# Kernel optimization log

Hardware: AMD Instinct MI355X
Metric: run time of the kernel (lower is better)

## Reference

```python
import jax, jax.numpy as jnp
import numpy as np

N = 100000
E = 1600000
EMB = 256
D = 128
B = 4096
L = 50
NCLASS = 10


def _spmm(edge_src, edge_dst, edge_w, h):
    # adj @ h with adj given as weighted edge list (dst aggregates from src)
    msg = h[edge_src] * edge_w[:, None]          # [E, D]
    return jax.ops.segment_sum(msg, edge_dst, num_segments=h.shape[0])


def setup_inputs() -> dict:
    key = jax.random.key(0)
    ks = jax.random.split(key, 20)
    inp = {}
    inp["A1_tensor"] = jax.random.normal(ks[0], (N, EMB), dtype=jnp.float32)
    inp["edge_src"] = jax.random.randint(ks[1], (E,), 0, N, dtype=jnp.int32)
    inp["edge_dst"] = jax.random.randint(ks[2], (E,), 0, N, dtype=jnp.int32)
    inp["edge_w"] = jax.random.uniform(ks[3], (E,), dtype=jnp.float32)
    inp["batch_idx"] = jax.random.randint(ks[4], (B, 1, L), 0, N, dtype=jnp.int32)
    s = 0.05  # modest init scale for numerical sanity
    inp["w_gc1"] = jax.random.normal(ks[5], (EMB, D), dtype=jnp.float32) * s
    inp["b_gc1"] = jax.random.normal(ks[6], (D,), dtype=jnp.float32) * s
    inp["w_gc2"] = jax.random.normal(ks[7], (D, D), dtype=jnp.float32) * s
    inp["b_gc2"] = jax.random.normal(ks[8], (D,), dtype=jnp.float32) * s
    inp["n_param"] = jax.random.uniform(ks[9], (N, 1), dtype=jnp.float32)
    inp["Lin1"] = jax.random.normal(ks[10], (EMB, D), dtype=jnp.float32) * s
    inp["Lin1_bias"] = jax.random.normal(ks[11], (D,), dtype=jnp.float32) * s
    inp["weight2"] = jax.random.normal(ks[12], (D, 64), dtype=jnp.float32) * s
    inp["bias2"] = jax.random.normal(ks[13], (64,), dtype=jnp.float32) * s
    inp["lin1_w"] = jax.random.normal(ks[14], ((L + 1) * 64, D), dtype=jnp.float32) * s
    inp["lin1_b"] = jax.random.normal(ks[15], (D,), dtype=jnp.float32) * s
    inp["classifier"] = jax.random.normal(ks[16], (D, NCLASS), dtype=jnp.float32) * s
    inp["classifier_bias"] = jax.random.normal(ks[17], (NCLASS,), dtype=jnp.float32) * s
    return inp


def reference(A1_tensor, edge_src, edge_dst, edge_w, batch_idx,
              w_gc1, b_gc1, w_gc2, b_gc2, n_param, Lin1, Lin1_bias,
              weight2, bias2, lin1_w, lin1_b, classifier, classifier_bias):
    # eval mode: both dropouts are identity
    a0 = A1_tensor @ Lin1 + Lin1_bias              # [N, D]
    a1 = a0 * n_param                              # per-node convex gate
    x1 = _spmm(edge_src, edge_dst, edge_w, A1_tensor @ w_gc1 + b_gc1)  # gc1
    x1 = a1 + x1 * (1.0 - n_param)
    x2 = _spmm(edge_src, edge_dst, edge_w, x1 @ w_gc2 + b_gc2)         # gc2
    bidx = batch_idx[:, 0, :]                      # [B, L]
    sel = x2[bidx]                                 # [B, L, D] irregular gather
    sel = jnp.concatenate([sel, jnp.sum(sel, axis=1, keepdims=True)], axis=1)  # [B, L+1, D]
    sel = jnp.einsum('bld,de->ble', sel, weight2) + bias2                      # [B, L+1, 64]
    sel = sel.reshape(bidx.shape[0], -1)           # [B, (L+1)*64]
    sel = sel @ lin1_w + lin1_b                    # [B, D]
    pre = sel @ classifier + classifier_bias       # [B, nclass]
    return (jnp.argmax(pre, axis=-1), sel)
```

## Files before the change

kernel.cpp:

```cpp
#include <hip/hip_runtime.h>
#include <cstdint>

#define NN   100000
#define EE   1600000
#define EMBD 256
#define DD   128
#define BBB  4096
#define LLL  50
#define NCLS 10

#define NB   196
#define BSH  9
#define EPB  4096

#define FIXS 1048576.0f
#define INVS (1.0f / 1048576.0f)

typedef __attribute__((ext_vector_type(8))) short bf16x8;
typedef __attribute__((ext_vector_type(4))) float f32x4;

__device__ __forceinline__ ushort f2bf(float f) {
  uint32_t u = __float_as_uint(f);
  u += 0x7fffu + ((u >> 16) & 1u);
  return (ushort)(u >> 16);
}
__device__ __forceinline__ float bf2f(ushort h) {
  return __uint_as_float(((uint32_t)h) << 16);
}

template<int BM, int BN, int BK, int TM, int TN>
__global__ __launch_bounds__(256)
void gemm_f32(const float* __restrict__ Av, int lda,
              const float* __restrict__ W, int ldw,
              const float* __restrict__ bias,
              float* __restrict__ Cv, int ldc,
              int M, int ktot, int kper,
              const int* __restrict__ bidxg,
              const float* __restrict__ Sg)
{
  constexpr int TX = BN / TN;
  constexpr int TY = BM / TM;
  static_assert(TX * TY == 256, "thread mapping");
  static_assert(TN % 4 == 0, "epilogue uses 4-wide vectors");
  constexpr int AQ = BK / 4;
  constexpr int ALOADS = (BM * AQ) / 256;
  static_assert((BM * AQ) % 256 == 0, "A-tile load mapping");
  constexpr int WQ4 = BN / 4;
  constexpr int WLOADS = (BK * WQ4) / 256;
  static_assert((BK * WQ4) % 256 == 0, "W-tile load mapping");

  __shared__ float As[BK][BM + 4];
  __shared__ float Ws[BK][BN];

  const int tid = threadIdx.x;
  const int tx = tid % TX, ty = tid / TX;
  const int bm0 = blockIdx.x * BM;
  const int bn0 = blockIdx.y * BN;
  const int z = blockIdx.z;
  const int koff = z * kper;
  int kc = ktot - koff; if (kc > kper) kc = kper;
  W += bn0 + (size_t)koff * ldw;
  Cv += (size_t)z * (size_t)M * ldc;
  const float* biasp = bias ? bias + bn0 : nullptr;

  float acc[TM][TN];
#pragma unroll
  for (int i = 0; i < TM; ++i)
#pragma unroll
    for (int j = 0; j < TN; ++j) acc[i][j] = 0.f;

  for (int kt = 0; kt < kc; kt += BK) {
#pragma unroll
    for (int p = 0; p < ALOADS; ++p) {
      int f = tid + p * 256;
      int row = f / AQ, q = f % AQ;
      int arow = bm0 + row;
      float4 av = make_float4(0.f, 0.f, 0.f, 0.f);
      if (arow < M) {
        if (bidxg) {
          int k = koff + kt + (q << 2);
          int l = k >> 6, jj = k & 63;
          const float* ap = (l < LLL)
              ? (Av + (size_t)bidxg[arow * LLL + l] * 64 + jj)
              : (Sg + (size_t)arow * 64 + jj);
          av = *(const float4*)ap;
        } else {
          av = *(const float4*)(Av + (long long)arow * lda + koff + kt + (q << 2));
        }
      }
      As[(q << 2) + 0][row] = av.x;
      As[(q << 2) + 1][row] = av.y;
      As[(q << 2) + 2][row] = av.z;
      As[(q << 2) + 3][row] = av.w;
    }
#pragma unroll
    for (int p = 0; p < WLOADS; ++p) {
      int f = tid + p * 256;
      int krow = f / WQ4, c4 = f % WQ4;
      *(float4*)&Ws[krow][c4 << 2] =
          *(const float4*)(W + (long long)(kt + krow) * ldw + (c4 << 2));
    }
    __syncthreads();
#pragma unroll
    for (int kk = 0; kk < BK; ++kk) {
      float a[TM], b[TN];
      if constexpr (TM % 4 == 0) {
#pragma unroll
        for (int i = 0; i < TM; i += 4)
          *(float4*)&a[i] = *(const float4*)&As[kk][ty * TM + i];
      } else {
#pragma unroll
        for (int i = 0; i < TM; ++i) a[i] = As[kk][ty * TM + i];
      }
#pragma unroll
      for (int j = 0; j < TN; j += 4)
        *(float4*)&b[j] = *(const float4*)&Ws[kk][tx * TN + j];
#pragma unroll
      for (int i = 0; i < TM; ++i)
#pragma unroll
        for (int j = 0; j < TN; ++j)
          acc[i][j] = fmaf(a[i], b[j], acc[i][j]);
    }
    __syncthreads();
  }

#pragma unroll
  for (int i = 0; i < TM; ++i) {
    int r = bm0 + ty * TM + i;
    if (r >= M) continue;
#pragma unroll
    for (int j4 = 0; j4 < TN; j4 += 4) {
      float4 v = make_float4(acc[i][j4], acc[i][j4 + 1],
                             acc[i][j4 + 2], acc[i][j4 + 3]);
      if (biasp != nullptr) {
        v.x += biasp[tx * TN + j4 + 0]; v.y += biasp[tx * TN + j4 + 1];
        v.z += biasp[tx * TN + j4 + 2]; v.w += biasp[tx * TN + j4 + 3];
      }
      *(float4*)(Cv + (long long)r * ldc + bn0 + tx * TN + j4) = v;
    }
  }
}

__global__ __launch_bounds__(256)
void gemm_qp_mfma(const float* __restrict__ A1,
                  const ushort* __restrict__ Wfh,
                  const ushort* __restrict__ Wfl,
                  const float* __restrict__ bab,
                  float* __restrict__ Qb, float* __restrict__ Pb, int M)
{
  __shared__ ushort LAh[64][32];
  __shared__ ushort LAl[64][32];
  const int tid = threadIdx.x;
  const int w = tid >> 6, l = tid & 63;
  const int bm0 = blockIdx.x * 64;
  const int srow = tid >> 2, skg = tid & 3;
  const int frow = (w << 4) + (l & 15);
  const int fk   = (l >> 4) << 3;

  f32x4 acc[8];
#pragma unroll
  for (int c = 0; c < 8; ++c) acc[c] = (f32x4){0.f, 0.f, 0.f, 0.f};

  for (int kt8 = 0; kt8 < 8; ++kt8) {
    {
      int grow = bm0 + srow;
      float x[8];
      if (grow < M) {
        const float* ap = A1 + (size_t)grow * 256 + (kt8 << 5) + (skg << 3);
        *(float4*)&x[0] = *(const float4*)ap;
        *(float4*)&x[4] = *(const float4*)(ap + 4);
      } else {
#pragma unroll
        for (int j = 0; j < 8; ++j) x[j] = 0.f;
      }
      ushort h[8], lo[8];
#pragma unroll
      for (int j = 0; j < 8; ++j) {
        h[j] = f2bf(x[j]);
        lo[j] = f2bf(x[j] - bf2f(h[j]));
      }
      *(bf16x8*)&LAh[srow][skg << 3] = *(bf16x8*)h;
      *(bf16x8*)&LAl[srow][skg << 3] = *(bf16x8*)lo;
    }
    __syncthreads();

    bf16x8 ah = *(const bf16x8*)&LAh[frow][fk];
    bf16x8 al = *(const bf16x8*)&LAl[frow][fk];
#pragma unroll
    for (int ct = 0; ct < 8; ++ct) {
      size_t off = ((size_t)((kt8 << 3) + ct) * 64 + l) << 3;
      bf16x8 bh = *(const bf16x8*)(Wfh + off);
      bf16x8 bl = *(const bf16x8*)(Wfl + off);
      acc[ct] = __builtin_amdgcn_mfma_f32_16x16x32_bf16(ah, bh, acc[ct], 0, 0, 0);
      acc[ct] = __builtin_amdgcn_mfma_f32_16x16x32_bf16(ah, bl, acc[ct], 0, 0, 0);
      acc[ct] = __builtin_amdgcn_mfma_f32_16x16x32_bf16(al, bh, acc[ct], 0, 0, 0);
    }
    __syncthreads();
  }

  const int r0 = bm0 + (w << 4) + ((l >> 4) << 2);
#pragma unroll
  for (int ct = 0; ct < 8; ++ct) {
    int gcol = (ct << 4) + (l & 15);
    float bia = bab[gcol];
    float* dst = (gcol < 64) ? (Qb + gcol) : (Pb + (gcol - 64));
#pragma unroll
    for (int r = 0; r < 4; ++r) {
      int grow = r0 + r;
      if (grow < M) dst[(size_t)grow * 64] = acc[ct][r] + bia;
    }
  }
}

__global__ __launch_bounds__(256)
void wfrag_k(const float* __restrict__ Wab, ushort* __restrict__ Wfh,
             ushort* __restrict__ Wfl)
{
  int t = blockIdx.x * 256 + threadIdx.x;
  if (t >= 4096) return;
  int f = t >> 6, l = t & 63;
  int kt = f >> 3, ct = f & 7;
  int row0 = (kt << 5) + ((l >> 4) << 3);
  int col = (ct << 4) + (l & 15);
  ushort h[8], lo[8];
#pragma unroll
  for (int j = 0; j < 8; ++j) {
    float x = Wab[(row0 + j) * 128 + col];
    h[j] = f2bf(x);
    lo[j] = f2bf(x - bf2f(h[j]));
  }
  size_t off = ((size_t)t) << 3;
  *(bf16x8*)(Wfh + off) = *(bf16x8*)h;
  *(bf16x8*)(Wfl + off) = *(bf16x8*)lo;
}

__global__ __launch_bounds__(256)
void fuse1_k(const float* __restrict__ wgc1, const float* __restrict__ lin1,
             const float* __restrict__ bgc1, const float* __restrict__ lin1b,
             const float* __restrict__ wgc2,
             float* __restrict__ T1, float* __restrict__ T2,
             float* __restrict__ ta, float* __restrict__ tb)
{
  int t = blockIdx.x * 256 + threadIdx.x;
  const float* Arow; float* outp; int n;
  if (t < 32768)      { n = t & 127; Arow = wgc1 + (t >> 7) * 128; outp = T1 + t; }
  else if (t < 65536) { int u = t - 32768; n = u & 127; Arow = lin1 + (u >> 7) * 128; outp = T2 + u; }
  else if (t < 65664) { n = t - 65536; Arow = bgc1;  outp = ta + n; }
  else if (t < 65792) { n = t - 65664; Arow = lin1b; outp = tb + n; }
  else return;
  float s = 0.f;
  for (int k = 0; k < 128; ++k) s = fmaf(Arow[k], wgc2[k * 128 + n], s);
  *outp = s;
}

__global__ __launch_bounds__(256)
void fuse2_k(const float* __restrict__ T1, const float* __restrict__ T2,
             const float* __restrict__ ta, const float* __restrict__ tb,
             const float* __restrict__ bgc2, const float* __restrict__ w2,
             float* __restrict__ Wab, float* __restrict__ bab,
             float* __restrict__ bcv)
{
  int t = blockIdx.x * 256 + threadIdx.x;
  const float* Arow; float* outp; int j;
  if (t < 32768) {
    int c = t & 127; j = c & 63;
    Arow = (c < 64 ? T1 : T2) + (t >> 7) * 128;
    outp = Wab + t;
  } else if (t < 32896) {
    int c = t - 32768; j = c & 63; Arow = (c < 64) ? ta : tb; outp = bab + c;
  } else if (t < 32960) {
    j = t - 32896; Arow = bgc2; outp = bcv + j;
  } else return;
  float s = 0.f;
  for (int k = 0; k < 128; ++k) s = fmaf(Arow[k], w2[k * 64 + j], s);
  *outp = s;
}

__global__ __launch_bounds__(256)
void cnt_k(const int* __restrict__ edst, int* __restrict__ gbkt)
{
  __shared__ int l[NB];
  const int tid = threadIdx.x;
  for (int i = tid; i < NB; i += 256) l[i] = 0;
  __syncthreads();
  const int e0 = blockIdx.x * EPB;
  const int e1 = min(EE, e0 + EPB);
#pragma unroll
  for (int u = 0; u < 16; ++u) {
    int e = e0 + u * 256 + tid;
    if (e < e1) atomicAdd(&l[edst[e] >> BSH], 1);
  }
  __syncthreads();
  for (int i = tid; i < NB; i += 256)
    if (l[i]) atomicAdd(&gbkt[i], l[i]);
}

__global__ __launch_bounds__(256)
void scanB_k(const int* __restrict__ gbkt, int* __restrict__ bbase,
             int* __restrict__ gcur, int* __restrict__ rp)
{
  __shared__ int s[256];
  int t = threadIdx.x;
  int v = (t < NB) ? gbkt[t] : 0;
  s[t] = v;
  __syncthreads();
  for (int off = 1; off < 256; off <<= 1) {
    int u = (t >= off) ? s[t - off] : 0;
    __syncthreads();
    s[t] += u;
    __syncthreads();
  }
  if (t < NB) {
    int ex = s[t] - v;
    bbase[t] = ex;
    gcur[t] = ex;
  }
  if (t == 0) { bbase[NB] = EE; rp[NN] = EE; }
}

__global__ __launch_bounds__(256)
void bin_k(const int* __restrict__ edst, const int* __restrict__ esrc,
           const float* __restrict__ ew, int* __restrict__ gcur,
           int4* __restrict__ ebd)
{
  __shared__ int lcnt[NB];
  __shared__ int lbase[NB];
  const int tid = threadIdx.x;
  const int e0 = blockIdx.x * EPB;
  const int e1 = min(EE, e0 + EPB);
  for (int i = tid; i < NB; i += 256) lcnt[i] = 0;
  __syncthreads();
  int dv[16], sv[16], wv[16];
#pragma unroll
  for (int u = 0; u < 16; ++u) {
    int e = e0 + u * 256 + tid;
    if (e < e1) {
      dv[u] = edst[e];
      sv[u] = esrc[e];
      wv[u] = __float_as_int(ew[e]);
      atomicAdd(&lcnt[dv[u] >> BSH], 1);
    } else dv[u] = -1;
  }
  __syncthreads();
  for (int i = tid; i < NB; i += 256) {
    lbase[i] = atomicAdd(&gcur[i], lcnt[i]);
    lcnt[i] = 0;
  }
  __syncthreads();
#pragma unroll
  for (int u = 0; u < 16; ++u) {
    if (dv[u] >= 0) {
      int c = dv[u] >> BSH;
      int k = atomicAdd(&lcnt[c], 1);
      int4 p; p.x = dv[u]; p.y = sv[u]; p.z = wv[u]; p.w = 0;
      ebd[lbase[c] + k] = p;
    }
  }
}

__global__ __launch_bounds__(256)
void sort_k(const int4* __restrict__ ebd, const int* __restrict__ bbase,
            int* __restrict__ rp, int2* __restrict__ sw)
{
  __shared__ int hist[512];
  __shared__ int excl[512];
  __shared__ int s2[256];
  __shared__ int lcur[512];
  const int c = blockIdx.x;
  const int n0 = c << BSH;
  const int n1 = min(NN, n0 + 512);
  const int nn = n1 - n0;
  const int tid = threadIdx.x;
  for (int i = tid; i < 512; i += 256) { hist[i] = 0; lcur[i] = 0; }
  __syncthreads();
  const int b0 = bbase[c];
  const int b1 = bbase[c + 1];
  for (int i = b0 + tid; i < b1; i += 256)
    atomicAdd(&hist[ebd[i].x - n0], 1);
  __syncthreads();
  int a0 = hist[2 * tid], a1 = hist[2 * tid + 1];
  s2[tid] = a0 + a1;
  __syncthreads();
  for (int off = 1; off < 256; off <<= 1) {
    int u = (tid >= off) ? s2[tid - off] : 0;
    __syncthreads();
    s2[tid] += u;
    __syncthreads();
  }
  int pe = tid ? s2[tid - 1] : 0;
  excl[2 * tid] = pe;
  excl[2 * tid + 1] = pe + a0;
  if (2 * tid < nn)     rp[n0 + 2 * tid]     = b0 + pe;
  if (2 * tid + 1 < nn) rp[n0 + 2 * tid + 1] = b0 + pe + a0;
  __syncthreads();
  for (int i = b0 + tid; i < b1; i += 256) {
    int4 p = ebd[i];
    int li = p.x - n0;
    int k = atomicAdd(&lcur[li], 1);
    int2 q; q.x = p.y; q.y = p.z;
    sw[b0 + excl[li] + k] = q;
  }
}

template<int MODE>
__global__ __launch_bounds__(256)
void spmm64(const int* __restrict__ rp, const int2* __restrict__ sw,
            const float* __restrict__ Gf, float* __restrict__ xout,
            const float* __restrict__ bias, const float* __restrict__ npar,
            const float* __restrict__ Pb)
{
  int widx = blockIdx.x * 4 + (threadIdx.x >> 6);
  if (widx >= NN) return;
  int lane = threadIdx.x & 63;
  int e0 = rp[widx], e1 = rp[widx + 1];
  int acc = 0;
  int j = e0;
  for (; j + 8 <= e1; j += 8) {
    float gv[8], wv[8];
#pragma unroll
    for (int u = 0; u < 8; ++u) {
      int2 q = sw[j + u];
      wv[u] = __int_as_float(q.y);
      gv[u] = Gf[(size_t)q.x * 64 + lane];
    }
#pragma unroll
    for (int u = 0; u < 8; ++u)
      acc += __float2int_rn(gv[u] * wv[u] * FIXS);
  }
  for (; j < e1; ++j) {
    int2 q = sw[j];
    acc += __float2int_rn(Gf[(size_t)q.x * 64 + lane] *
                          __int_as_float(q.y) * FIXS);
  }
  float v = (float)acc * INVS;
  if (MODE == 1) {
    xout[(size_t)widx * 64 + lane] = v + bias[lane];
  } else {
    float nv = npar[widx];
    float p = Pb[(size_t)widx * 64 + lane];
    xout[(size_t)widx * 64 + lane] = nv * p + (1.f - nv) * v + bias[lane];
  }
}

__global__ __launch_bounds__(256)
void sumS_k(const float* __restrict__ Z, const int* __restrict__ bidx,
            const float* __restrict__ b2, float* __restrict__ S)
{
  int wv = threadIdx.x >> 6;
  int lane = threadIdx.x & 63;
  int b = blockIdx.x * 4 + wv;
  if (b >= BBB) return;
  const int* bi = bidx + (size_t)b * LLL;
  float s = 0.f;
  for (int l = 0; l < LLL; ++l)
    s += Z[(size_t)bi[l] * 64 + lane];
  S[(size_t)b * 64 + lane] = s - 49.f * b2[lane];
}

__global__ __launch_bounds__(256)
void reduce4_k(const float* __restrict__ P4, const float* __restrict__ l1b,
               float* __restrict__ sel)
{
  int t = blockIdx.x * 256 + threadIdx.x;
  if (t >= BBB * 32) return;
  int r = t >> 5, c4 = t & 31;
  size_t off = (size_t)r * 128 + (c4 << 2);
  const size_t zs = (size_t)BBB * 128;
  float4 s0 = *(const float4*)(P4 + off);
  float4 s1 = *(const float4*)(P4 + zs + off);
  float4 s2 = *(const float4*)(P4 + 2 * zs + off);
  float4 s3 = *(const float4*)(P4 + 3 * zs + off);
  float4 b  = *(const float4*)(l1b + (c4 << 2));
  float4 o;
  o.x = ((s0.x + s1.x) + s2.x) + s3.x + b.x;
  o.y = ((s0.y + s1.y) + s2.y) + s3.y + b.y;
  o.z = ((s0.z + s1.z) + s2.z) + s3.z + b.z;
  o.w = ((s0.w + s1.w) + s2.w) + s3.w + b.w;
  *(float4*)(sel + off) = o;
}

__global__ __launch_bounds__(256)
void cls_k(const float* __restrict__ sel, const float* __restrict__ Wc,
           const float* __restrict__ bc, float* __restrict__ outIdx)
{
  int wv = threadIdx.x >> 6;
  int lane = threadIdx.x & 63;
  int b = blockIdx.x * 4 + wv;
  if (b >= BBB) return;
  float logit = -1e30f;
  if (lane < NCLS) {
    float s = bc[lane];
    const float* sr = sel + (size_t)b * DD;
    for (int d = 0; d < DD; ++d) s = fmaf(sr[d], Wc[d * NCLS + lane], s);
    logit = s;
  }
  float best = -1e30f; int bi = 0;
  for (int c = 0; c < NCLS; ++c) {
    float v = __shfl(logit, c, 64);
    if (v > best) { best = v; bi = c; }
  }
  if (lane == 0) outIdx[b] = (float)bi;
}

extern "C" void kernel_launch(void* const* d_in, const int* in_sizes, int n_in,
                              void* d_out, int out_size, void* d_ws, size_t ws_size,
                              hipStream_t stream)
{
  const float* A1    = (const float*)d_in[0];
  const int*   esrc  = (const int*)d_in[1];
  const int*   edst  = (const int*)d_in[2];
  const float* ew    = (const float*)d_in[3];
  const int*   bidx  = (const int*)d_in[4];
  const float* wgc1  = (const float*)d_in[5];
  const float* bgc1  = (const float*)d_in[6];
  const float* wgc2  = (const float*)d_in[7];
  const float* bgc2  = (const float*)d_in[8];
  const float* npar  = (const float*)d_in[9];
  const float* lin1  = (const float*)d_in[10];
  const float* lin1b = (const float*)d_in[11];
  const float* w2    = (const float*)d_in[12];
  const float* b2    = (const float*)d_in[13];
  const float* l1w   = (const float*)d_in[14];
  const float* l1b   = (const float*)d_in[15];
  const float* clsw  = (const float*)d_in[16];
  const float* clsb  = (const float*)d_in[17];

  float* out = (float*)d_out;
  float* sel = out + BBB;

  uint8_t* ws   = (uint8_t*)d_ws;
  int4*    ebd  = (int4*) (ws);
  float*   Qb   = (float*)(ws);
  float*   Z    = (float*)(ws);
  float*   Pb   = (float*)(ws + 25600000);
  float*   G    = (float*)(ws + 51200000);
  float*   P4   = (float*)(ws + 51200000);
  int2*    sw   = (int2*) (ws + 76800000);
  int*     rp   = (int*)  (ws + 89600000);
  int*     gbkt = (int*)  (ws + 90000016);
  int*     gcur = (int*)  (ws + 90001040);
  int*     bbase= (int*)  (ws + 90002064);
  float*   S    = (float*)(ws + 90400528);
  float*   T1   = (float*)(ws + 91449104);
  float*   T2   = (float*)(ws + 91580176);
  float*   Wab  = (float*)(ws + 91711248);
  float*   ta   = (float*)(ws + 91842320);
  float*   tb   = (float*)(ws + 91842832);
  float*   bab  = (float*)(ws + 91843344);
  float*   bcv  = (float*)(ws + 91843856);
  ushort*  Wfh  = (ushort*)(ws + 91844112);
  ushort*  Wfl  = (ushort*)(ws + 91909648);

  dim3 blk(256);
  const int gEB = (EE + EPB - 1) / EPB;

  hipLaunchKernelGGL(fuse1_k, dim3(257), blk, 0, stream,
      wgc1, lin1, bgc1, lin1b, wgc2, T1, T2, ta, tb);
  hipLaunchKernelGGL(fuse2_k, dim3(129), blk, 0, stream,
      T1, T2, ta, tb, bgc2, w2, Wab, bab, bcv);
  hipLaunchKernelGGL(wfrag_k, dim3(16), blk, 0, stream, Wab, Wfh, Wfl);

  hipMemsetAsync(gbkt, 0, NB * 4, stream);
  hipLaunchKernelGGL(cnt_k, dim3(gEB), blk, 0, stream, edst, gbkt);
  hipLaunchKernelGGL(scanB_k, dim3(1), blk, 0, stream, gbkt, bbase, gcur, rp);
  hipLaunchKernelGGL(bin_k, dim3(gEB), blk, 0, stream, edst, esrc, ew, gcur, ebd);
  hipLaunchKernelGGL(sort_k, dim3(NB), blk, 0, stream, ebd, bbase, rp, sw);

  hipLaunchKernelGGL(gemm_qp_mfma, dim3(1563), blk, 0, stream,
      A1, Wfh, Wfl, bab, Qb, Pb, NN);

  hipLaunchKernelGGL((spmm64<2>), dim3(NN / 4), blk, 0, stream,
      rp, sw, Qb, G, bcv, npar, Pb);

  hipLaunchKernelGGL((spmm64<1>), dim3(NN / 4), blk, 0, stream,
      rp, sw, G, Z, b2, (const float*)nullptr, (const float*)nullptr);

  hipLaunchKernelGGL(sumS_k, dim3(BBB / 4), blk, 0, stream, Z, bidx, b2, S);

  hipLaunchKernelGGL((gemm_f32<32,64,32,2,4>), dim3(BBB / 32, 2, 4), blk, 0, stream,
      Z, 64, l1w, DD, (const float*)nullptr, P4, DD,
      BBB, (LLL + 1) * 64, 13 * 64, bidx, S);

  hipLaunchKernelGGL(reduce4_k, dim3(BBB * 32 / 256), blk, 0, stream, P4, l1b, sel);

  hipLaunchKernelGGL(cls_k, dim3(BBB / 4), blk, 0, stream, sel, clsw, clsb, out);
}
```

Baseline: 376.7 us.

## Load GEMM A fragments directly to registers and retile split-K head GEMM

New measurement: 381.2 us. No clear change (+1.2%).

```diff
diff --git a/kernel.cpp b/kernel.cpp
--- a/kernel.cpp
+++ b/kernel.cpp
@@ -148,44 +148,35 @@
                   const float* __restrict__ bab,
                   float* __restrict__ Qb, float* __restrict__ Pb, int M)
 {
-  __shared__ ushort LAh[64][32];
-  __shared__ ushort LAl[64][32];
   const int tid = threadIdx.x;
   const int w = tid >> 6, l = tid & 63;
-  const int bm0 = blockIdx.x * 64;
-  const int srow = tid >> 2, skg = tid & 3;
-  const int frow = (w << 4) + (l & 15);
-  const int fk   = (l >> 4) << 3;
+  const int fk = (l >> 4) << 3;
+  const int r0 = blockIdx.x * 64 + (w << 4);
+  const int grow = r0 + (l & 15);
+  const bool rok = grow < M;
+  const float* aptr = A1 + (size_t)grow * 256 + fk;
 
   f32x4 acc[8];
 #pragma unroll
   for (int c = 0; c < 8; ++c) acc[c] = (f32x4){0.f, 0.f, 0.f, 0.f};
 
   for (int kt8 = 0; kt8 < 8; ++kt8) {
-    {
-      int grow = bm0 + srow;
-      float x[8];
-      if (grow < M) {
-        const float* ap = A1 + (size_t)grow * 256 + (kt8 << 5) + (skg << 3);
-        *(float4*)&x[0] = *(const float4*)ap;
-        *(float4*)&x[4] = *(const float4*)(ap + 4);
-      } else {
-#pragma unroll
-        for (int j = 0; j < 8; ++j) x[j] = 0.f;
-      }
-      ushort h[8], lo[8];
-#pragma unroll
-      for (int j = 0; j < 8; ++j) {
-        h[j] = f2bf(x[j]);
-        lo[j] = f2bf(x[j] - bf2f(h[j]));
-      }
-      *(bf16x8*)&LAh[srow][skg << 3] = *(bf16x8*)h;
-      *(bf16x8*)&LAl[srow][skg << 3] = *(bf16x8*)lo;
-    }
-    __syncthreads();
-
-    bf16x8 ah = *(const bf16x8*)&LAh[frow][fk];
-    bf16x8 al = *(const bf16x8*)&LAl[frow][fk];
+    float x[8];
+    if (rok) {
+      *(float4*)&x[0] = *(const float4*)(aptr + (kt8 << 5));
+      *(float4*)&x[4] = *(const float4*)(aptr + (kt8 << 5) + 4);
+    } else {
+#pragma unroll
+      for (int j = 0; j < 8; ++j) x[j] = 0.f;
+    }
+    ushort h[8], lo[8];
+#pragma unroll
+    for (int j = 0; j < 8; ++j) {
+      h[j] = f2bf(x[j]);
+      lo[j] = f2bf(x[j] - bf2f(h[j]));
+    }
+    bf16x8 ah = *(bf16x8*)h;
+    bf16x8 al = *(bf16x8*)lo;
 #pragma unroll
     for (int ct = 0; ct < 8; ++ct) {
       size_t off = ((size_t)((kt8 << 3) + ct) * 64 + l) << 3;
@@ -195,10 +186,9 @@
       acc[ct] = __builtin_amdgcn_mfma_f32_16x16x32_bf16(ah, bl, acc[ct], 0, 0, 0);
       acc[ct] = __builtin_amdgcn_mfma_f32_16x16x32_bf16(al, bh, acc[ct], 0, 0, 0);
     }
-    __syncthreads();
-  }
-
-  const int r0 = bm0 + (w << 4) + ((l >> 4) << 2);
+  }
+
+  const int er0 = r0 + ((l >> 4) << 2);
 #pragma unroll
   for (int ct = 0; ct < 8; ++ct) {
     int gcol = (ct << 4) + (l & 15);
@@ -206,8 +196,8 @@
     float* dst = (gcol < 64) ? (Qb + gcol) : (Pb + (gcol - 64));
 #pragma unroll
     for (int r = 0; r < 4; ++r) {
-      int grow = r0 + r;
-      if (grow < M) dst[(size_t)grow * 64] = acc[ct][r] + bia;
+      int grw = er0 + r;
+      if (grw < M) dst[(size_t)grw * 64] = acc[ct][r] + bia;
     }
   }
 }
@@ -458,7 +448,7 @@
 }
 
 __global__ __launch_bounds__(256)
-void reduce4_k(const float* __restrict__ P4, const float* __restrict__ l1b,
+void reduce8_k(const float* __restrict__ P8, const float* __restrict__ l1b,
                float* __restrict__ sel)
 {
   int t = blockIdx.x * 256 + threadIdx.x;
@@ -466,16 +456,14 @@
   int r = t >> 5, c4 = t & 31;
   size_t off = (size_t)r * 128 + (c4 << 2);
   const size_t zs = (size_t)BBB * 128;
-  float4 s0 = *(const float4*)(P4 + off);
-  float4 s1 = *(const float4*)(P4 + zs + off);
-  float4 s2 = *(const float4*)(P4 + 2 * zs + off);
-  float4 s3 = *(const float4*)(P4 + 3 * zs + off);
-  float4 b  = *(const float4*)(l1b + (c4 << 2));
-  float4 o;
-  o.x = ((s0.x + s1.x) + s2.x) + s3.x + b.x;
-  o.y = ((s0.y + s1.y) + s2.y) + s3.y + b.y;
-  o.z = ((s0.z + s1.z) + s2.z) + s3.z + b.z;
-  o.w = ((s0.w + s1.w) + s2.w) + s3.w + b.w;
+  float4 o = *(const float4*)(P8 + off);
+#pragma unroll
+  for (int z = 1; z < 8; ++z) {
+    float4 s = *(const float4*)(P8 + z * zs + off);
+    o.x += s.x; o.y += s.y; o.z += s.z; o.w += s.w;
+  }
+  float4 b = *(const float4*)(l1b + (c4 << 2));
+  o.x += b.x; o.y += b.y; o.z += b.z; o.w += b.w;
   *(float4*)(sel + off) = o;
 }
 
@@ -534,7 +522,7 @@
   float*   Z    = (float*)(ws);
   float*   Pb   = (float*)(ws + 25600000);
   float*   G    = (float*)(ws + 51200000);
-  float*   P4   = (float*)(ws + 51200000);
+  float*   P8   = (float*)(ws + 51200000);
   int2*    sw   = (int2*) (ws + 76800000);
   int*     rp   = (int*)  (ws + 89600000);
   int*     gbkt = (int*)  (ws + 90000016);
@@ -566,7 +554,7 @@
   hipLaunchKernelGGL(bin_k, dim3(gEB), blk, 0, stream, edst, esrc, ew, gcur, ebd);
   hipLaunchKernelGGL(sort_k, dim3(NB), blk, 0, stream, ebd, bbase, rp, sw);
 
-  hipLaunchKernelGGL(gemm_qp_mfma, dim3(1563), blk, 0, stream,
+  hipLaunchKernelGGL(gemm_qp_mfma, dim3((NN + 63) / 64), blk, 0, stream,
       A1, Wfh, Wfl, bab, Qb, Pb, NN);
 
   hipLaunchKernelGGL((spmm64<2>), dim3(NN / 4), blk, 0, stream,
@@ -577,11 +565,11 @@
 
   hipLaunchKernelGGL(sumS_k, dim3(BBB / 4), blk, 0, stream, Z, bidx, b2, S);
 
-  hipLaunchKernelGGL((gemm_f32<32,64,32,2,4>), dim3(BBB / 32, 2, 4), blk, 0, stream,
-      Z, 64, l1w, DD, (const float*)nullptr, P4, DD,
-      BBB, (LLL + 1) * 64, 13 * 64, bidx, S);
-
-  hipLaunchKernelGGL(reduce4_k, dim3(BBB * 32 / 256), blk, 0, stream, P4, l1b, sel);
+  hipLaunchKernelGGL((gemm_f32<64,64,32,4,4>), dim3(BBB / 64, 2, 8), blk, 0, stream,
+      Z, 64, l1w, DD, (const float*)nullptr, P8, DD,
+      BBB, (LLL + 1) * 64, 13 * 32, bidx, S);
+
+  hipLaunchKernelGGL(reduce8_k, dim3(BBB * 32 / 256), blk, 0, stream, P8, l1b, sel);
 
   hipLaunchKernelGGL(cls_k, dim3(BBB / 4), blk, 0, stream, sel, clsw, clsb, out);
 }
```
